# Kernel tuning notes

Measured on AMD Instinct MI355X. Metric: run time of the kernel, lower is better.

## Reference

```python
import jax, jax.numpy as jnp
import numpy as np

D_MODEL = 2048
D_INNER = 2048          # expand=1
N_HEADS = 32            # n_qk_heads == n_v_heads
D_STATE = 64
HEADDIM = D_INNER // N_HEADS  # 64
D_CONV = 4
CHUNK = 128
D_FF = 8192
EPS = 1e-5
CONV_DIM = D_INNER + 2 * N_HEADS * D_STATE            # 6144
D_IN_PROJ = 2 * D_INNER + 2 * N_HEADS * D_STATE + N_HEADS  # 8224


def rmsnorm(x, w, eps=EPS):
    x32 = x.astype(jnp.float32)
    x32 = x32 * jax.lax.rsqrt(jnp.mean(x32 * x32, axis=-1, keepdims=True) + eps)
    return (w * x32).astype(x.dtype)


def causal_conv1d(x, w, b):
    # x: (B, L, C), w: (C, K) depthwise, b: (C,). Causal left padding (K-1).
    K = w.shape[1]
    y = jax.lax.conv_general_dilated(
        x, jnp.transpose(w)[:, None, :],  # (K, 1, C)
        window_strides=(1,), padding=[(K - 1, 0)],
        dimension_numbers=("NWC", "WIO", "NWC"),
        feature_group_count=x.shape[-1])
    return y + b


def ssd_scan(x, dt, Bm, Cm, chunk=CHUNK):
    # Discrete Mamba2 SSD: h_t = exp(-softplus(dt_t)) * h_{t-1} + B_t (x) x_t; y_t = C_t . h_t
    # x: (b,l,h,p), dt: (b,l,h), Bm/Cm: (b,l,h,n)
    b, l, h, p = x.shape
    n = Bm.shape[-1]
    c = l // chunk
    xr = x.reshape(b, c, chunk, h, p)
    a_log = (-jax.nn.softplus(dt)).reshape(b, c, chunk, h)  # per-step log decay
    Br = Bm.reshape(b, c, chunk, h, n)
    Cr = Cm.reshape(b, c, chunk, h, n)
    cum = jnp.cumsum(a_log, axis=2)  # inclusive cumulative log-decay within chunk (b,c,q,h)
    # intra-chunk: scores[i,j] = exp(cum_i - cum_j) * (C_i . B_j), causal j <= i
    seg = jnp.exp(cum[:, :, :, None, :] - cum[:, :, None, :, :])       # (b,c,i,j,h)
    cb = jnp.einsum("bcihn,bcjhn->bcijh", Cr, Br)
    mask = jnp.tril(jnp.ones((chunk, chunk), bool))
    scores = jnp.where(mask[None, None, :, :, None], seg * cb, 0.0)
    y_intra = jnp.einsum("bcijh,bcjhp->bcihp", scores, xr)
    # per-chunk end state contribution
    decay_to_end = jnp.exp(cum[:, :, -1:, :] - cum)                     # (b,c,q,h)
    S = jnp.einsum("bcqh,bcqhn,bcqhp->bchnp", decay_to_end, Br, xr)
    A_chunk = jnp.exp(cum[:, :, -1, :])                                  # (b,c,h)
    def step(hprev, inp):
        Ac, Sc = inp
        return Ac[..., None, None] * hprev + Sc, hprev
    h0 = jnp.zeros((b, h, n, p), x.dtype)
    _, Hprev = jax.lax.scan(step, h0, (jnp.moveaxis(A_chunk, 1, 0), jnp.moveaxis(S, 1, 0)))
    Hprev = jnp.moveaxis(Hprev, 0, 1)  # state at each chunk start (b,c,h,n,p)
    y_inter = jnp.einsum("bcqh,bcqhn,bchnp->bcqhp", jnp.exp(cum), Cr, Hprev)
    return (y_intra + y_inter).reshape(b, l, h, p)


def mixer(u, in_proj_w, z_bias, conv_w, conv_b, D, out_proj_w):
    b, l, _ = u.shape
    zxbcdt = u @ in_proj_w.T  # (b,l,8224)
    z = zxbcdt[..., :D_INNER]
    xBC = zxbcdt[..., D_INNER:D_INNER + CONV_DIM]
    dt = zxbcdt[..., D_INNER + CONV_DIM:]  # (b,l,H)
    xBC = causal_conv1d(xBC, conv_w, conv_b)  # activation = identity
    x = xBC[..., :D_INNER].reshape(b, l, N_HEADS, HEADDIM)
    Bm = xBC[..., D_INNER:D_INNER + N_HEADS * D_STATE].reshape(b, l, N_HEADS, D_STATE)
    Cm = xBC[..., D_INNER + N_HEADS * D_STATE:].reshape(b, l, N_HEADS, D_STATE)
    y = ssd_scan(x, dt, Bm, Cm)
    y = y + D[None, None, :, None] * x  # D skip
    y = y.reshape(b, l, D_INNER)
    return (y * jax.nn.silu(z + z_bias)) @ out_proj_w.T


def setup_inputs() -> dict:
    key = jax.random.key(0)
    ks = jax.random.split(key, 8)
    s = 0.02
    return {
        "hidden_states": jax.random.normal(ks[0], (2, 2048, D_MODEL), jnp.float32),
        "in_proj_w": jax.random.normal(ks[1], (D_IN_PROJ, D_MODEL), jnp.float32) * s,
        "z_bias": jnp.zeros((D_INNER,), jnp.float32),
        "conv_w": jax.random.normal(ks[2], (CONV_DIM, D_CONV), jnp.float32) * s,
        "conv_b": jnp.zeros((CONV_DIM,), jnp.float32),
        "D": jnp.ones((N_HEADS,), jnp.float32),
        "out_proj_w": jax.random.normal(ks[3], (D_MODEL, D_INNER), jnp.float32) * s,
        "norm1_w": jnp.ones((D_MODEL,), jnp.float32),
        "norm2_w": jnp.ones((D_MODEL,), jnp.float32),
        "gate_w": jax.random.normal(ks[4], (D_FF, D_MODEL), jnp.float32) * s,
        "up_w": jax.random.normal(ks[5], (D_FF, D_MODEL), jnp.float32) * s,
        "down_w": jax.random.normal(ks[6], (D_MODEL, D_FF), jnp.float32) * s,
    }


def reference(hidden_states, in_proj_w, z_bias, conv_w, conv_b, D, out_proj_w,
              norm1_w, norm2_w, gate_w, up_w, down_w):
    residual = hidden_states
    h = rmsnorm(hidden_states, norm1_w)
    h = mixer(h, in_proj_w, z_bias, conv_w, conv_b, D, out_proj_w) + residual
    residual = h
    h = rmsnorm(h, norm2_w)
    h = (jax.nn.silu(h @ gate_w.T) * (h @ up_w.T)) @ down_w.T  # LlamaMLP
    return residual + h
```

## Files before the change

### kernel.cpp

```cpp
#include <hip/hip_runtime.h>


typedef unsigned short u16;
typedef __bf16 bf16x8 __attribute__((ext_vector_type(8)));
typedef float f32x4 __attribute__((ext_vector_type(4)));

#define D_MODEL   2048
#define D_INNER   2048
#define NH        32
#define CONV_DIM  6144
#define D_IN_PROJ 8224
#define DFF       8192
#define BATCH     2
#define SEQ       2048
#define M_TOK     4096
#define NCHUNK    16
#define CHUNK     128

__device__ __forceinline__ u16 f2b(float f) {
  union { float f; unsigned int u; } v; v.f = f;
  unsigned int r = v.u + 0x7FFFu + ((v.u >> 16) & 1u);
  return (u16)(r >> 16);
}
__device__ __forceinline__ float b2f(u16 u) {
  union { unsigned int u; float f; } v; v.u = ((unsigned int)u) << 16; return v.f;
}

__device__ __forceinline__ void async16(const void* g, void* l) {
  __builtin_amdgcn_global_load_lds((const __attribute__((address_space(1))) void*)g,
                                   (__attribute__((address_space(3))) void*)l, 16, 0, 0);
}

template <int EPI, int BM>
__global__ void __launch_bounds__(512, 2) gemm8(
    const u16* __restrict__ A, const u16* __restrict__ W,
    float* Cf, u16* Cb, const float* __restrict__ auxf, float* Fdt,
    int K, int Nbound, int ldC, int GN, int WR) {
  constexpr int RB = BM / 32;
  constexpr int CA = BM / 128;
  constexpr int LPT = CA + 2;
  constexpr int SLOT_A = BM * 32;
  constexpr int SLOT_B = 256 * 32;
  __shared__ __align__(16) u16 sA[4 * SLOT_A];
  __shared__ __align__(16) u16 sB[4 * SLOT_B];

  const int tid = threadIdx.x;
  const int lane = tid & 63, wave = tid >> 6;

  const int nwg = gridDim.x;
  const int q = nwg >> 3, r = nwg & 7, xc = blockIdx.x & 7, jj = blockIdx.x >> 3;
  const int wg = (xc < r ? xc * (q + 1) : r * (q + 1) + (xc - r) * q) + jj;
  const int bm = wg / GN, bn = wg % GN;

  const int wrow = (wave >> 2) * (BM / 2);
  const int wcol = (wave & 3) * 64;

  const int l2 = lane >> 2;
  const int cbl = (lane & 3) ^ ((lane >> 3) & 3);
  const u16* pa[CA];
  const u16* pb[2];
#pragma unroll
  for (int i = 0; i < CA; ++i)
    pa[i] = A + (size_t)(bm * BM + (wave * CA + i) * 16 + l2) * K + cbl * 8;
#pragma unroll
  for (int i = 0; i < 2; ++i) {
    int br = bn * 256 + (wave * 2 + i) * 16 + l2;
    if (br >= WR) br = 0;
    pb[i] = W + (size_t)br * K + cbl * 8;
  }

  auto stageA = [&](int slot) {
#pragma unroll
    for (int i = 0; i < CA; ++i) {
      async16(pa[i], &sA[slot * SLOT_A + (wave * CA + i) * 512 + lane * 8]);
      pa[i] += 32;
    }
  };
  auto stageB = [&](int slot) {
#pragma unroll
    for (int i = 0; i < 2; ++i) {
      async16(pb[i], &sB[slot * SLOT_B + (wave * 2 + i) * 512 + lane * 8]);
      pb[i] += 32;
    }
  };

  const int lr = lane & 15;
  const int afo = lr * 32 + ((((lane >> 4) ^ ((lr >> 1) & 3))) << 3);

  f32x4 acc[RB][4];
  const f32x4 z4 = {0.f, 0.f, 0.f, 0.f};
#pragma unroll
  for (int m = 0; m < RB; ++m)
#pragma unroll
    for (int n = 0; n < 4; ++n) acc[m][n] = z4;

  const int NT = K >> 5;
  stageA(0); stageB(0);
  stageA(1); stageB(1);
  asm volatile("s_waitcnt vmcnt(%0)" :: "n"(LPT) : "memory");
  __builtin_amdgcn_s_barrier();
  __builtin_amdgcn_sched_barrier(0);

  for (int t = 0; t < NT; ++t) {
    const int slot = t & 3;
    const int s2 = (t + 2) & 3;
    const bool pf = (t + 2 < NT);
    const u16* sAs = &sA[slot * SLOT_A + wrow * 32 + afo];
    const u16* sBs = &sB[slot * SLOT_B + wcol * 32 + afo];
    bf16x8 av[4], bv[4];
#pragma unroll
    for (int m = 0; m < 4; ++m) av[m] = *(const bf16x8*)(sAs + m * 512);
#pragma unroll
    for (int n = 0; n < 4; ++n) bv[n] = *(const bf16x8*)(sBs + n * 512);
    if (pf) stageA(s2);
    if constexpr (RB == 4) { if (pf) stageB(s2); }
    __builtin_amdgcn_s_barrier();
    asm volatile("s_waitcnt lgkmcnt(0)" ::: "memory");
    __builtin_amdgcn_sched_barrier(0);
    __builtin_amdgcn_s_setprio(1);
#pragma unroll
    for (int m = 0; m < 4; ++m)
#pragma unroll
      for (int n = 0; n < 4; ++n)
        acc[m][n] = __builtin_amdgcn_mfma_f32_16x16x32_bf16(av[m], bv[n], acc[m][n], 0, 0, 0);
    __builtin_amdgcn_s_setprio(0);
    if constexpr (RB == 8) {
      __builtin_amdgcn_s_barrier();
      __builtin_amdgcn_sched_barrier(0);
#pragma unroll
      for (int m = 0; m < 4; ++m) av[m] = *(const bf16x8*)(sAs + (m + 4) * 512);
      if (pf) stageB(s2);
      __builtin_amdgcn_s_barrier();
      asm volatile("s_waitcnt lgkmcnt(0)" ::: "memory");
      __builtin_amdgcn_sched_barrier(0);
      __builtin_amdgcn_s_setprio(1);
#pragma unroll
      for (int m = 0; m < 4; ++m)
#pragma unroll
        for (int n = 0; n < 4; ++n)
          acc[m + 4][n] = __builtin_amdgcn_mfma_f32_16x16x32_bf16(av[m], bv[n], acc[m + 4][n], 0, 0, 0);
      __builtin_amdgcn_s_setprio(0);
    }
    if (pf) { asm volatile("s_waitcnt vmcnt(%0)" :: "n"(LPT) : "memory"); }
    else    { asm volatile("s_waitcnt vmcnt(0)" ::: "memory"); }
    __builtin_amdgcn_s_barrier();
    __builtin_amdgcn_sched_barrier(0);
  }

  const int er = (lane >> 4) * 4, ec = lane & 15;
  const int bmb = bm * BM + wrow, bnb = bn * 256 + wcol;
  if constexpr (EPI == 6) {
#pragma unroll
    for (int m = 0; m < RB; ++m)
#pragma unroll
      for (int rr = 0; rr < 4; ++rr) {
        const size_t grow = bmb + m * 16 + er + rr;
#pragma unroll
        for (int n = 0; n < 4; n += 2) {
          const int oc = ((bnb + n * 16) >> 5) * 16 + ec;
          const float g = acc[m][n][rr], u = acc[m][n + 1][rr];
          const float sg = 1.f / (1.f + __expf(-g));
          Cb[grow * DFF + oc] = f2b(u * g * sg);
        }
      }
  } else {
#pragma unroll
    for (int m = 0; m < RB; ++m)
#pragma unroll
      for (int rr = 0; rr < 4; ++rr) {
        const int grow = bmb + m * 16 + er + rr;
#pragma unroll
        for (int n = 0; n < 4; ++n) {
          const int gcol = bnb + n * 16 + ec;
          if (gcol < Nbound) {
            const float v = acc[m][n][rr];
            if constexpr (EPI == 1) {
              const size_t idx = (size_t)grow * ldC + gcol;
              Cf[idx] = v + auxf[idx];
            } else if constexpr (EPI == 4) {
              Cb[(size_t)grow * ldC + gcol] = f2b(v);
            } else if constexpr (EPI == 5) {
              Fdt[(size_t)grow * NH + gcol] = v;
            }
          }
        }
      }
  }
}

__global__ void cvt_kernel(const float* __restrict__ s, u16* __restrict__ d, int n4) {
  const int i = blockIdx.x * 256 + threadIdx.x;
  if (i >= n4) return;
  const float4 v = ((const float4*)s)[i];
  ushort4 r;
  r.x = f2b(v.x); r.y = f2b(v.y); r.z = f2b(v.z); r.w = f2b(v.w);
  ((ushort4*)d)[i] = r;
}

__global__ void cvt_gateup_kernel(const float* __restrict__ g, const float* __restrict__ u,
                                  u16* __restrict__ d) {
  const int i = blockIdx.x * 256 + threadIdx.x;
  const int total = 2 * DFF * D_MODEL / 4;
  if (i >= total) return;
  const int rowlen4 = D_MODEL / 4;
  const int vrow = i / rowlen4, c4 = i % rowlen4;
  const bool isg = vrow < DFF;
  const int sr = isg ? vrow : vrow - DFF;
  const float4 v = ((const float4*)(isg ? g : u))[(size_t)sr * rowlen4 + c4];
  const int dr = (sr >> 4) * 32 + (isg ? 0 : 16) + (sr & 15);
  ushort4 rr; rr.x = f2b(v.x); rr.y = f2b(v.y); rr.z = f2b(v.z); rr.w = f2b(v.w);
  ((ushort4*)d)[(size_t)dr * rowlen4 + c4] = rr;
}

__global__ void rmsnorm_kernel(const float* __restrict__ x, const float* __restrict__ w,
                               u16* __restrict__ o) {
  const int row = blockIdx.x;
  const float* xr = x + (size_t)row * D_MODEL;
  float ss = 0.f;
  for (int c = threadIdx.x; c < D_MODEL; c += 256) { const float v = xr[c]; ss += v * v; }
#pragma unroll
  for (int off = 32; off > 0; off >>= 1) ss += __shfl_down(ss, off, 64);
  __shared__ float red[4];
  if ((threadIdx.x & 63) == 0) red[threadIdx.x >> 6] = ss;
  __syncthreads();
  const float scale = rsqrtf((red[0] + red[1] + red[2] + red[3]) * (1.f / D_MODEL) + 1e-5f);
  u16* orow = o + (size_t)row * D_MODEL;
  for (int c = threadIdx.x; c < D_MODEL; c += 256) orow[c] = f2b(xr[c] * scale * w[c]);
}

__global__ void conv_kernel(const u16* __restrict__ zx, const float* __restrict__ cw,
                            const float* __restrict__ cb, u16* __restrict__ out) {
  const int idx = blockIdx.x * 256 + threadIdx.x;
  const int ch = idx % CONV_DIM;
  const int m = idx / CONV_DIM;
  const int l = m & (SEQ - 1);
  float accv = cb[ch];
#pragma unroll
  for (int k = 0; k < 4; ++k) {
    const int ls = l - 3 + k;
    if (ls >= 0) accv += cw[ch * 4 + k] * b2f(zx[(size_t)(m - 3 + k) * D_IN_PROJ + D_INNER + ch]);
  }
  out[idx] = f2b(accv);
}

__global__ void dtcum_kernel(const float* __restrict__ dtbuf, float* __restrict__ cum) {
  const int blk = blockIdx.x;
  const int h = blk & 31, cc = (blk >> 5) & 15, b = blk >> 9;
  const int i = threadIdx.x;
  const int m = b * SEQ + cc * CHUNK + i;
  const float dt = dtbuf[(size_t)m * NH + h];
  const float sp = (dt > 20.f) ? dt : log1pf(__expf(dt));
  __shared__ float s[128];
  s[i] = -sp;
  __syncthreads();
  for (int off = 1; off < 128; off <<= 1) {
    const float v = (i >= off) ? s[i - off] : 0.f;
    __syncthreads();
    s[i] += v;
    __syncthreads();
  }
  cum[(size_t)m * NH + h] = s[i];
}

__global__ void state_kernel(const u16* __restrict__ xbc, const float* __restrict__ cum,
                             float* __restrict__ S) {
  const int blk = blockIdx.x;
  const int h = blk & 31, cc = (blk >> 5) & 15, b = blk >> 9;
  const int m0 = b * SEQ + cc * CHUNK;
  const int tid = threadIdx.x;
  const int tp = tid & 63, tg = tid >> 6;
  const int n0 = tg * 16;
  const float cl = cum[(size_t)(m0 + 127) * NH + h];
  __shared__ float sBq[32][64], sxq[32][64], sd[32];
  float accv[16];
#pragma unroll
  for (int i = 0; i < 16; ++i) accv[i] = 0.f;
  for (int q0 = 0; q0 < 128; q0 += 32) {
    __syncthreads();
    for (int e = tid; e < 2048; e += 256) {
      const int q = e >> 6, col = e & 63;
      const size_t rowb = (size_t)(m0 + q0 + q) * CONV_DIM;
      sBq[q][col] = b2f(xbc[rowb + D_INNER + h * 64 + col]);
      sxq[q][col] = b2f(xbc[rowb + h * 64 + col]);
    }
    if (tid < 32) sd[tid] = __expf(cl - cum[(size_t)(m0 + q0 + tid) * NH + h]);
    __syncthreads();
    for (int q = 0; q < 32; ++q) {
      const float xv = sxq[q][tp] * sd[q];
#pragma unroll
      for (int i = 0; i < 16; ++i) accv[i] += sBq[q][n0 + i] * xv;
    }
  }
  float* Sp = S + (((size_t)(b * 16 + cc) * NH + h) * 64) * 64;
#pragma unroll
  for (int i = 0; i < 16; ++i) Sp[(size_t)(n0 + i) * 64 + tp] = accv[i];
}

__global__ void scan_kernel(const float* __restrict__ S, const float* __restrict__ cum,
                            float* __restrict__ H) {
  const int idx = blockIdx.x * 256 + threadIdx.x;
  const int p = idx & 63, n = (idx >> 6) & 63, h = (idx >> 12) & 31, b = idx >> 17;
  float hs = 0.f;
  for (int cc = 0; cc < NCHUNK; ++cc) {
    const size_t off = (((size_t)(b * 16 + cc) * NH + h) * 64 + n) * 64 + p;
    H[off] = hs;
    const float Ac = __expf(cum[(size_t)(b * SEQ + cc * CHUNK + 127) * NH + h]);
    hs = Ac * hs + S[off];
  }
}

#define SPITCH 136
#define CPITCH 72
__global__ void __launch_bounds__(256, 2) y_kernel(
    const u16* __restrict__ xbc, const float* __restrict__ cum,
    const float* __restrict__ H, const float* __restrict__ Dp,
    const u16* __restrict__ zx, const float* __restrict__ zb,
    u16* __restrict__ yo) {
  const int blk = blockIdx.x;
  const int h = blk & 31, cc = (blk >> 5) & 15, b = blk >> 9;
  const int m0 = b * SEQ + cc * CHUNK;
  const int tid = threadIdx.x;
  const int lane = tid & 63, wave = tid >> 6;

  __shared__ __align__(16) u16 sC[128 * CPITCH];
  __shared__ __align__(16) u16 sU[64 * SPITCH + 64 * CPITCH];
  __shared__ __align__(16) u16 sP[128 * SPITCH];
  __shared__ float sCum[128];
  u16* sB = sU;
  u16* sxT = sU;
  u16* sHT = sU + 64 * SPITCH;

  {
    const int i = tid >> 4, n4 = (tid & 15) * 4;
    for (int i0 = 0; i0 < 128; i0 += 16) {
      const size_t g = (size_t)(m0 + i0 + i) * CONV_DIM + h * 64 + n4;
      *(ushort4*)&sC[(i0 + i) * CPITCH + n4] = *(const ushort4*)&xbc[g + 2 * D_INNER];
      *(ushort4*)&sB[(i0 + i) * CPITCH + n4] = *(const ushort4*)&xbc[g + D_INNER];
    }
    if (tid < 128) sCum[tid] = cum[(size_t)(m0 + tid) * NH + h];
  }
  __syncthreads();

  const int lr = lane & 15;
  const int lk = (lane >> 4) * 8;
  const int er = (lane >> 4) * 4;
  const int ec = lane & 15;

  {
    const int R = (wave >> 1) * 64, Cq = (wave & 1) * 64;
    const f32x4 z4 = {0.f, 0.f, 0.f, 0.f};
    f32x4 acc[4][4];
#pragma unroll
    for (int i = 0; i < 4; ++i)
#pragma unroll
      for (int j = 0; j < 4; ++j) acc[i][j] = z4;
#pragma unroll
    for (int k0 = 0; k0 < 64; k0 += 32) {
      bf16x8 af[4], bfv[4];
#pragma unroll
      for (int mi = 0; mi < 4; ++mi)
        af[mi] = *(const bf16x8*)&sC[(R + mi * 16 + lr) * CPITCH + k0 + lk];
#pragma unroll
      for (int ni = 0; ni < 4; ++ni)
        bfv[ni] = *(const bf16x8*)&sB[(Cq + ni * 16 + lr) * CPITCH + k0 + lk];
#pragma unroll
      for (int mi = 0; mi < 4; ++mi)
#pragma unroll
        for (int ni = 0; ni < 4; ++ni)
          acc[mi][ni] = __builtin_amdgcn_mfma_f32_16x16x32_bf16(af[mi], bfv[ni], acc[mi][ni], 0, 0, 0);
    }
#pragma unroll
    for (int mi = 0; mi < 4; ++mi)
#pragma unroll
      for (int r = 0; r < 4; ++r) {
        const int row = R + mi * 16 + er + r;
#pragma unroll
        for (int ni = 0; ni < 4; ++ni) {
          const int col = Cq + ni * 16 + ec;
          const float pv = (row >= col) ? __expf(sCum[row] - sCum[col]) * acc[mi][ni][r] : 0.f;
          sP[row * SPITCH + col] = f2b(pv);
        }
      }
  }
  __syncthreads();

  {
    const int i = tid >> 1, n32 = (tid & 1) * 32;
    const float sc = __expf(sCum[i]);
    for (int n = n32; n < n32 + 32; ++n)
      sC[i * CPITCH + n] = f2b(b2f(sC[i * CPITCH + n]) * sc);
  }
  {
    const int j = tid >> 1, p32 = (tid & 1) * 32;
    const size_t g = (size_t)(m0 + j) * CONV_DIM + h * 64;
    for (int p = p32; p < p32 + 32; ++p)
      sxT[p * SPITCH + j] = xbc[g + p];
    const float* Hp = H + (((size_t)(b * 16 + cc) * NH + h) * 64) * 64;
    if (j < 64) {
      const int n = j;
      for (int p = p32; p < p32 + 32; ++p)
        sHT[p * CPITCH + n] = f2b(Hp[n * 64 + p]);
    }
  }
  __syncthreads();

  {
    const int R2 = wave * 32;
    const f32x4 z4 = {0.f, 0.f, 0.f, 0.f};
    f32x4 acc[2][4];
#pragma unroll
    for (int i = 0; i < 2; ++i)
#pragma unroll
      for (int j = 0; j < 4; ++j) acc[i][j] = z4;
#pragma unroll
    for (int k0 = 0; k0 < 128; k0 += 32) {
      bf16x8 af[2], bfv[4];
#pragma unroll
      for (int mi = 0; mi < 2; ++mi)
        af[mi] = *(const bf16x8*)&sP[(R2 + mi * 16 + lr) * SPITCH + k0 + lk];
#pragma unroll
      for (int ni = 0; ni < 4; ++ni)
        bfv[ni] = *(const bf16x8*)&sxT[(ni * 16 + lr) * SPITCH + k0 + lk];
#pragma unroll
      for (int mi = 0; mi < 2; ++mi)
#pragma unroll
        for (int ni = 0; ni < 4; ++ni)
          acc[mi][ni] = __builtin_amdgcn_mfma_f32_16x16x32_bf16(af[mi], bfv[ni], acc[mi][ni], 0, 0, 0);
    }
#pragma unroll
    for (int k0 = 0; k0 < 64; k0 += 32) {
      bf16x8 af[2], bfv[4];
#pragma unroll
      for (int mi = 0; mi < 2; ++mi)
        af[mi] = *(const bf16x8*)&sC[(R2 + mi * 16 + lr) * CPITCH + k0 + lk];
#pragma unroll
      for (int ni = 0; ni < 4; ++ni)
        bfv[ni] = *(const bf16x8*)&sHT[(ni * 16 + lr) * CPITCH + k0 + lk];
#pragma unroll
      for (int mi = 0; mi < 2; ++mi)
#pragma unroll
        for (int ni = 0; ni < 4; ++ni)
          acc[mi][ni] = __builtin_amdgcn_mfma_f32_16x16x32_bf16(af[mi], bfv[ni], acc[mi][ni], 0, 0, 0);
    }
    const float Dh = Dp[h];
#pragma unroll
    for (int mi = 0; mi < 2; ++mi)
#pragma unroll
      for (int r = 0; r < 4; ++r) {
        const int row = R2 + mi * 16 + er + r;
        const int m = m0 + row;
#pragma unroll
        for (int ni = 0; ni < 4; ++ni) {
          const int p = ni * 16 + ec;
          const int gc = h * 64 + p;
          const float xv = b2f(sxT[p * SPITCH + row]);
          const float z = b2f(zx[(size_t)m * D_IN_PROJ + gc]) + zb[gc];
          const float sg = 1.f / (1.f + __expf(-z));
          yo[(size_t)m * D_INNER + gc] = f2b((acc[mi][ni][r] + Dh * xv) * z * sg);
        }
      }
  }
}

extern "C" void kernel_launch(void* const* d_in, const int* in_sizes, int n_in,
                              void* d_out, int out_size, void* d_ws, size_t ws_size,
                              hipStream_t stream) {
  (void)in_sizes; (void)n_in; (void)out_size; (void)ws_size;
  const float* hidden = (const float*)d_in[0];
  const float* w_in   = (const float*)d_in[1];
  const float* z_bias = (const float*)d_in[2];
  const float* conv_w = (const float*)d_in[3];
  const float* conv_b = (const float*)d_in[4];
  const float* Dp     = (const float*)d_in[5];
  const float* w_out  = (const float*)d_in[6];
  const float* n1w    = (const float*)d_in[7];
  const float* n2w    = (const float*)d_in[8];
  const float* w_g    = (const float*)d_in[9];
  const float* w_u    = (const float*)d_in[10];
  const float* w_d    = (const float*)d_in[11];
  float* out = (float*)d_out;

  char* p = (char*)d_ws;
  auto take = [&](size_t bytes) { char* r = p; p += (bytes + 255) & ~(size_t)255; return r; };
  u16*   Bzx  = (u16*)take((size_t)M_TOK * D_IN_PROJ * 2);
  u16*   Bxbc = (u16*)take((size_t)M_TOK * CONV_DIM * 2);
  float* F_cum = (float*)take((size_t)M_TOK * NH * 4);
  float* F_S   = (float*)take((size_t)BATCH * NCHUNK * NH * 64 * 64 * 4);
  float* F_H   = (float*)take((size_t)BATCH * NCHUNK * NH * 64 * 64 * 4);
  u16*   B_h   = (u16*)take((size_t)M_TOK * D_MODEL * 2);
  float* F_dt  = (float*)take((size_t)M_TOK * NH * 4);
  u16*   W_buf = (u16*)take((size_t)D_IN_PROJ * D_MODEL * 2);
  u16* B_y  = (u16*)F_S;
  u16* W_gu = Bzx;
  u16* B_gu = Bxbc;

  const int c2 = (D_MODEL * D_INNER / 4 + 255) / 256;
  const int c8 = (DFF * D_MODEL / 4 + 255) / 256;

  cvt_kernel<<<(D_IN_PROJ * D_MODEL / 4 + 255) / 256, 256, 0, stream>>>(w_in, W_buf, D_IN_PROJ * D_MODEL / 4);
  rmsnorm_kernel<<<M_TOK, 256, 0, stream>>>(hidden, n1w, B_h);
  gemm8<4, 256><<<16 * 32, 512, 0, stream>>>(B_h, W_buf, nullptr, Bzx, nullptr, nullptr,
                                             D_MODEL, 8192, D_IN_PROJ, 32, 8192);
  gemm8<5, 128><<<32, 512, 0, stream>>>(B_h, W_buf + (size_t)8192 * D_MODEL, nullptr, nullptr,
                                        nullptr, F_dt, D_MODEL, NH, 0, 1, 32);

  conv_kernel<<<M_TOK * CONV_DIM / 256, 256, 0, stream>>>(Bzx, conv_w, conv_b, Bxbc);
  dtcum_kernel<<<BATCH * NCHUNK * NH, 128, 0, stream>>>(F_dt, F_cum);
  state_kernel<<<BATCH * NCHUNK * NH, 256, 0, stream>>>(Bxbc, F_cum, F_S);
  scan_kernel<<<BATCH * NH * 64 * 64 / 256, 256, 0, stream>>>(F_S, F_cum, F_H);
  y_kernel<<<BATCH * NCHUNK * NH, 256, 0, stream>>>(Bxbc, F_cum, F_H, Dp, Bzx, z_bias, B_y);

  cvt_kernel<<<c2, 256, 0, stream>>>(w_out, W_buf, D_MODEL * D_INNER / 4);
  gemm8<1, 128><<<32 * 8, 512, 0, stream>>>(B_y, W_buf, out, nullptr, hidden, nullptr,
                                            D_INNER, D_MODEL, D_MODEL, 8, 2048);

  rmsnorm_kernel<<<M_TOK, 256, 0, stream>>>(out, n2w, B_h);
  cvt_gateup_kernel<<<2 * DFF * D_MODEL / 4 / 256, 256, 0, stream>>>(w_g, w_u, W_gu);
  gemm8<6, 256><<<16 * 64, 512, 0, stream>>>(B_h, W_gu, nullptr, B_gu, nullptr, nullptr,
                                             D_MODEL, 2 * DFF, 0, 64, 16384);
  cvt_kernel<<<c8, 256, 0, stream>>>(w_d, W_buf, D_MODEL * DFF / 4);
  gemm8<1, 128><<<32 * 8, 512, 0, stream>>>(B_gu, W_buf, out, nullptr, out,
                                            nullptr, DFF, D_MODEL, D_MODEL, 8, 2048);
}
```

Before: 1.165 ms.

## Deepen GEMM LDS pipeline with register double-buffered fragments and grouped tile order

Restructures the gemm8 main loop into a 4-way unrolled pipeline. Three LDS slots are prefetched ahead instead of two, fragments are double-buffered in registers so the next tile's LDS reads overlap the current MFMAs, and the per-iteration split barriers for RB==8 are removed. It also remaps workgroup IDs so groups of four M-tiles share an N column, aiming for better L2 reuse of weights. Holding full RB fragment sets twice raises register pressure, which could hurt occupancy at launch bounds (512,2) or cause spills. The wait count LPT was not changed even though three stages are now in flight.

After: 1.092 ms. 1.07x faster.

```diff
diff --git a/kernel.cpp b/kernel.cpp
--- a/kernel.cpp
+++ b/kernel.cpp
@@ -41,8 +41,10 @@
   constexpr int LPT = CA + 2;
   constexpr int SLOT_A = BM * 32;
   constexpr int SLOT_B = 256 * 32;
-  __shared__ __align__(16) u16 sA[4 * SLOT_A];
-  __shared__ __align__(16) u16 sB[4 * SLOT_B];
+  __shared__ __align__(16) u16 sA0[SLOT_A], sA1[SLOT_A], sA2[SLOT_A], sA3[SLOT_A];
+  __shared__ __align__(16) u16 sB0[SLOT_B], sB1[SLOT_B], sB2[SLOT_B], sB3[SLOT_B];
+  u16* const slA[4] = {sA0, sA1, sA2, sA3};
+  u16* const slB[4] = {sB0, sB1, sB2, sB3};
 
   const int tid = threadIdx.x;
   const int lane = tid & 63, wave = tid >> 6;
@@ -50,7 +52,8 @@
   const int nwg = gridDim.x;
   const int q = nwg >> 3, r = nwg & 7, xc = blockIdx.x & 7, jj = blockIdx.x >> 3;
   const int wg = (xc < r ? xc * (q + 1) : r * (q + 1) + (xc - r) * q) + jj;
-  const int bm = wg / GN, bn = wg % GN;
+  const int gm = wg / (4 * GN), rm = wg % (4 * GN);
+  const int bm = gm * 4 + (rm & 3), bn = rm >> 2;
 
   const int wrow = (wave >> 2) * (BM / 2);
   const int wcol = (wave & 3) * 64;
@@ -69,17 +72,15 @@
     pb[i] = W + (size_t)br * K + cbl * 8;
   }
 
-  auto stageA = [&](int slot) {
+  auto stageAB = [&](u16* sa, u16* sb) {
 #pragma unroll
     for (int i = 0; i < CA; ++i) {
-      async16(pa[i], &sA[slot * SLOT_A + (wave * CA + i) * 512 + lane * 8]);
+      async16(pa[i], sa + (wave * CA + i) * 512 + lane * 8);
       pa[i] += 32;
     }
-  };
-  auto stageB = [&](int slot) {
 #pragma unroll
     for (int i = 0; i < 2; ++i) {
-      async16(pb[i], &sB[slot * SLOT_B + (wave * 2 + i) * 512 + lane * 8]);
+      async16(pb[i], sb + (wave * 2 + i) * 512 + lane * 8);
       pb[i] += 32;
     }
   };
@@ -87,6 +88,15 @@
   const int lr = lane & 15;
   const int afo = lr * 32 + ((((lane >> 4) ^ ((lr >> 1) & 3))) << 3);
 
+  auto rdFrags = [&](const u16* sa, const u16* sb, bf16x8 (&fa)[RB], bf16x8 (&fb)[4]) {
+    const u16* ap = sa + wrow * 32 + afo;
+    const u16* bp = sb + wcol * 32 + afo;
+#pragma unroll
+    for (int m = 0; m < RB; ++m) fa[m] = *(const bf16x8*)(ap + m * 512);
+#pragma unroll
+    for (int n = 0; n < 4; ++n) fb[n] = *(const bf16x8*)(bp + n * 512);
+  };
+
   f32x4 acc[RB][4];
   const f32x4 z4 = {0.f, 0.f, 0.f, 0.f};
 #pragma unroll
@@ -94,58 +104,58 @@
 #pragma unroll
     for (int n = 0; n < 4; ++n) acc[m][n] = z4;
 
+  auto doMFMA = [&](bf16x8 (&fa)[RB], bf16x8 (&fb)[4]) {
+    __builtin_amdgcn_s_setprio(1);
+#pragma unroll
+    for (int m = 0; m < RB; ++m)
+#pragma unroll
+      for (int n = 0; n < 4; ++n)
+        acc[m][n] = __builtin_amdgcn_mfma_f32_16x16x32_bf16(fa[m], fb[n], acc[m][n], 0, 0, 0);
+    __builtin_amdgcn_s_setprio(0);
+  };
+
+#define BOUNDARY(cond)                                                         \
+  if (cond) { asm volatile("s_waitcnt vmcnt(%0)" :: "n"(LPT) : "memory"); }    \
+  else      { asm volatile("s_waitcnt vmcnt(0)" ::: "memory"); }               \
+  __builtin_amdgcn_s_barrier();                                                \
+  __builtin_amdgcn_sched_barrier(0);
+
   const int NT = K >> 5;
-  stageA(0); stageB(0);
-  stageA(1); stageB(1);
+  stageAB(slA[0], slB[0]);
+  stageAB(slA[1], slB[1]);
+  stageAB(slA[2], slB[2]);
   asm volatile("s_waitcnt vmcnt(%0)" :: "n"(LPT) : "memory");
   __builtin_amdgcn_s_barrier();
   __builtin_amdgcn_sched_barrier(0);
 
-  for (int t = 0; t < NT; ++t) {
-    const int slot = t & 3;
-    const int s2 = (t + 2) & 3;
-    const bool pf = (t + 2 < NT);
-    const u16* sAs = &sA[slot * SLOT_A + wrow * 32 + afo];
-    const u16* sBs = &sB[slot * SLOT_B + wcol * 32 + afo];
-    bf16x8 av[4], bv[4];
-#pragma unroll
-    for (int m = 0; m < 4; ++m) av[m] = *(const bf16x8*)(sAs + m * 512);
-#pragma unroll
-    for (int n = 0; n < 4; ++n) bv[n] = *(const bf16x8*)(sBs + n * 512);
-    if (pf) stageA(s2);
-    if constexpr (RB == 4) { if (pf) stageB(s2); }
-    __builtin_amdgcn_s_barrier();
-    asm volatile("s_waitcnt lgkmcnt(0)" ::: "memory");
-    __builtin_amdgcn_sched_barrier(0);
-    __builtin_amdgcn_s_setprio(1);
-#pragma unroll
-    for (int m = 0; m < 4; ++m)
-#pragma unroll
-      for (int n = 0; n < 4; ++n)
-        acc[m][n] = __builtin_amdgcn_mfma_f32_16x16x32_bf16(av[m], bv[n], acc[m][n], 0, 0, 0);
-    __builtin_amdgcn_s_setprio(0);
-    if constexpr (RB == 8) {
-      __builtin_amdgcn_s_barrier();
-      __builtin_amdgcn_sched_barrier(0);
-#pragma unroll
-      for (int m = 0; m < 4; ++m) av[m] = *(const bf16x8*)(sAs + (m + 4) * 512);
-      if (pf) stageB(s2);
-      __builtin_amdgcn_s_barrier();
-      asm volatile("s_waitcnt lgkmcnt(0)" ::: "memory");
-      __builtin_amdgcn_sched_barrier(0);
-      __builtin_amdgcn_s_setprio(1);
-#pragma unroll
-      for (int m = 0; m < 4; ++m)
-#pragma unroll
-        for (int n = 0; n < 4; ++n)
-          acc[m + 4][n] = __builtin_amdgcn_mfma_f32_16x16x32_bf16(av[m], bv[n], acc[m + 4][n], 0, 0, 0);
-      __builtin_amdgcn_s_setprio(0);
-    }
-    if (pf) { asm volatile("s_waitcnt vmcnt(%0)" :: "n"(LPT) : "memory"); }
-    else    { asm volatile("s_waitcnt vmcnt(0)" ::: "memory"); }
-    __builtin_amdgcn_s_barrier();
-    __builtin_amdgcn_sched_barrier(0);
-  }
+  bf16x8 fa0[RB], fb0[4], fa1[RB], fb1[4];
+  rdFrags(slA[0], slB[0], fa0, fb0);
+
+  for (int t = 0; t < NT; t += 4) {
+    if (t + 1 < NT) rdFrags(slA[1], slB[1], fa1, fb1);
+    if (t + 3 < NT) stageAB(slA[3], slB[3]);
+    doMFMA(fa0, fb0);
+    BOUNDARY(t + 3 < NT)
+    if (t + 1 < NT) {
+      if (t + 2 < NT) rdFrags(slA[2], slB[2], fa0, fb0);
+      if (t + 4 < NT) stageAB(slA[0], slB[0]);
+      doMFMA(fa1, fb1);
+      BOUNDARY(t + 4 < NT)
+    }
+    if (t + 2 < NT) {
+      if (t + 3 < NT) rdFrags(slA[3], slB[3], fa1, fb1);
+      if (t + 5 < NT) stageAB(slA[1], slB[1]);
+      doMFMA(fa0, fb0);
+      BOUNDARY(t + 5 < NT)
+    }
+    if (t + 3 < NT) {
+      if (t + 4 < NT) rdFrags(slA[0], slB[0], fa0, fb0);
+      if (t + 6 < NT) stageAB(slA[2], slB[2]);
+      doMFMA(fa1, fb1);
+      BOUNDARY(t + 6 < NT)
+    }
+  }
+#undef BOUNDARY
 
   const int er = (lane >> 4) * 4, ec = lane & 15;
   const int bmb = bm * BM + wrow, bnb = bn * 256 + wcol;
```
